# Kernel optimization log

Measured on AMD Instinct MI355X. Metric: run time of the kernel, lower is better.

## Reference

```python
import jax, jax.numpy as jnp
import numpy as np

D = 2048
N_EXPERTS = 64
K = 2


def setup_inputs() -> dict:
    key = jax.random.key(0)
    kx, kw = jax.random.split(key)
    x = jax.random.normal(kx, (4, 4096, D), dtype=jnp.float32)
    # xavier_uniform for Linear(d, n_experts): bound = sqrt(6/(fan_in+fan_out))
    bound = float(np.sqrt(6.0 / (D + N_EXPERTS)))
    W = jax.random.uniform(kw, (N_EXPERTS, D), dtype=jnp.float32, minval=-bound, maxval=bound)
    b = jnp.zeros((N_EXPERTS,), dtype=jnp.float32)
    return {"x": x, "W": W, "b": b}


def reference(x, W, b):
    # logits: [B, S, E]  (eval mode: no noise)
    logits = jnp.einsum("bsd,ed->bse", x, W) + b
    topk_vals, topk_idx = jax.lax.top_k(logits, K)  # [B, S, K]
    gates = jax.nn.softmax(topk_vals, axis=-1)
    return gates, topk_idx
```

## Files before the change

kernel.cpp:

```cpp
#include <hip/hip_runtime.h>
#include <math.h>

#define DD 2048
#define EE 64
#define TM 32
#define BK 64
#define NCHUNK (DD / BK)
#define THREADS 512

#define ROWB 272
#define XPLANE (TM * ROWB)
#define WPLANE (EE * ROWB)
#define BUFB   (XPLANE + WPLANE)

typedef _Float16 f16x8 __attribute__((ext_vector_type(8)));
typedef float    f32x4 __attribute__((ext_vector_type(4)));

#define BARRIER() { asm volatile("s_waitcnt lgkmcnt(0)" ::: "memory"); \
                    __builtin_amdgcn_s_barrier(); \
                    __builtin_amdgcn_sched_barrier(0); }

__device__ static inline void split8(const float4 a, const float4 b,
                                     f16x8& hi, f16x8& lo) {
    const float S = 32.f;
    const float v[8] = {a.x * S, a.y * S, a.z * S, a.w * S,
                        b.x * S, b.y * S, b.z * S, b.w * S};
#pragma unroll
    for (int i = 0; i < 8; ++i) {
        const _Float16 h = (_Float16)v[i];
        hi[i] = h;
        lo[i] = (_Float16)(v[i] - (float)h);
    }
}

__global__ __launch_bounds__(THREADS, 4) void router_kernel(
    const float* __restrict__ x, const float* __restrict__ W,
    const float* __restrict__ bias_g, float* __restrict__ out, int n_tokens)
{
    __shared__ __attribute__((aligned(16))) char  lds[2 * BUFB];
    __shared__ __attribute__((aligned(16))) float logits[TM * (EE + 1)];

    const int tid   = threadIdx.x;
    const int tBase = blockIdx.x * TM;

    const int sr = tid >> 3;
    const int sg = tid & 7;
    const bool do_x = (sr < TM);

    const float* xrow = x + (size_t)(tBase + (sr & (TM - 1))) * DD + sg * 8;
    const float* wrow = W + (size_t)sr * DD + sg * 8;

    float4 rxA0 = {0,0,0,0}, rxA1 = {0,0,0,0}, rwA0, rwA1;
    float4 rxB0 = {0,0,0,0}, rxB1 = {0,0,0,0}, rwB0, rwB1;

#define LOADS(c, rx0, rx1, rw0, rw1) { \
        rw0 = *(const float4*)&wrow[(c) * BK];       \
        rw1 = *(const float4*)&wrow[(c) * BK + 4];   \
        if (do_x) {                                  \
            rx0 = *(const float4*)&xrow[(c) * BK];   \
            rx1 = *(const float4*)&xrow[(c) * BK + 4]; } }

#define WRITE_STAGE(buf, rx0, rx1, rw0, rw1) { \
    char* base = lds + (size_t)(buf) * BUFB; \
    { f16x8 hi, lo; split8(rw0, rw1, hi, lo); \
      const int off = XPLANE + sr * ROWB + sg * 32; \
      *(f16x8*)(base + off)      = hi; \
      *(f16x8*)(base + off + 16) = lo; } \
    if (do_x) { f16x8 hi, lo; split8(rx0, rx1, hi, lo); \
      const int off = sr * ROWB + sg * 32; \
      *(f16x8*)(base + off)      = hi; \
      *(f16x8*)(base + off + 16) = lo; } }

    const int wv   = tid >> 6;
    const int lane = tid & 63;
    const int mt   = wv & 1;
    const int nt   = wv >> 1;
    const int r16  = lane & 15;
    const int kg   = lane >> 4;

    const int aoff = (mt * 16 + r16) * ROWB + kg * 32;
    const int boff = XPLANE + (nt * 16 + r16) * ROWB + kg * 32;

    f32x4 acc = {0.f, 0.f, 0.f, 0.f};

#define COMPUTE(buf) { \
    const char* base = lds + (size_t)(buf) * BUFB; \
    _Pragma("unroll") for (int ks = 0; ks < 2; ++ks) { \
        const f16x8 ah = *(const f16x8*)(base + aoff + ks * 128); \
        const f16x8 al = *(const f16x8*)(base + aoff + ks * 128 + 16); \
        const f16x8 bh = *(const f16x8*)(base + boff + ks * 128); \
        const f16x8 bl = *(const f16x8*)(base + boff + ks * 128 + 16); \
        acc = __builtin_amdgcn_mfma_f32_16x16x32_f16(ah, bh, acc, 0, 0, 0); \
        acc = __builtin_amdgcn_mfma_f32_16x16x32_f16(al, bh, acc, 0, 0, 0); \
        acc = __builtin_amdgcn_mfma_f32_16x16x32_f16(ah, bl, acc, 0, 0, 0); \
    } }

    LOADS(0, rxA0, rxA1, rwA0, rwA1);
    WRITE_STAGE(0, rxA0, rxA1, rwA0, rwA1);
    LOADS(1, rxB0, rxB1, rwB0, rwB1);

    for (int c = 0; c < NCHUNK; c += 2) {
        BARRIER();
        if (c + 2 < NCHUNK) LOADS(c + 2, rxA0, rxA1, rwA0, rwA1);
        COMPUTE(0);
        WRITE_STAGE(1, rxB0, rxB1, rwB0, rwB1);

        BARRIER();
        if (c + 3 < NCHUNK) LOADS(c + 3, rxB0, rxB1, rwB0, rwB1);
        COMPUTE(1);
        if (c + 2 < NCHUNK)
            WRITE_STAGE(0, rxA0, rxA1, rwA0, rwA1);
    }

    __syncthreads();
    const int col  = nt * 16 + r16;
    const float bcol = bias_g[col];
    const float INV  = 1.f / 1024.f;
    const int rbase  = mt * 16 + kg * 4;
#pragma unroll
    for (int r = 0; r < 4; ++r)
        logits[(rbase + r) * (EE + 1) + col] = acc[r] * INV + bcol;
    __syncthreads();

    if (tid < TM) {
        const float* lrow = &logits[tid * (EE + 1)];
        float v1 = -INFINITY, v2 = -INFINITY;
        int   i1 = 0, i2 = 0;
        for (int e = 0; e < EE; ++e) {
            const float v = lrow[e];
            if (v > v1) { v2 = v1; i2 = i1; v1 = v; i1 = e; }
            else if (v > v2) { v2 = v; i2 = e; }
        }
        const float ed  = expf(v2 - v1);
        const float inv = 1.f / (1.f + ed);
        const int tok = tBase + tid;
        out[tok * 2 + 0] = inv;
        out[tok * 2 + 1] = ed * inv;
        float* oidx = out + (size_t)2 * n_tokens;
        oidx[tok * 2 + 0] = (float)i1;
        oidx[tok * 2 + 1] = (float)i2;
    }
}

extern "C" void kernel_launch(void* const* d_in, const int* in_sizes, int n_in,
                              void* d_out, int out_size, void* d_ws, size_t ws_size,
                              hipStream_t stream) {
    const float* x = (const float*)d_in[0];
    const float* W = (const float*)d_in[1];
    const float* b = (const float*)d_in[2];
    float* out = (float*)d_out;

    const int n_tokens = in_sizes[0] / DD;
    const int n_blocks = n_tokens / TM;

    router_kernel<<<n_blocks, THREADS, 0, stream>>>(x, W, b, out, n_tokens);
}
```

Baseline: 202.8 us.

## Pre-split W into fp16 hi/lo in workspace and deepen load pipeline

A small pre-kernel converts W once per call into interleaved fp16 hi/lo pairs stored in the workspace. The router kernel then loads the pre-split W directly instead of re-splitting it in every block, and spreads the x loads across all 512 threads rather than half of them. The register pipeline also grows from two to three chunks in flight, with four barriers per iteration. The cost is an extra kernel launch and more registers, and the __syncthreads before the logits write is removed, which leans on the final barrier for ordering.

```diff
diff --git a/kernel.cpp b/kernel.cpp
--- a/kernel.cpp
+++ b/kernel.cpp
@@ -13,7 +13,10 @@
 #define WPLANE (EE * ROWB)
 #define BUFB   (XPLANE + WPLANE)
 
+#define WROWB 8192
+
 typedef _Float16 f16x8 __attribute__((ext_vector_type(8)));
+typedef _Float16 f16x4 __attribute__((ext_vector_type(4)));
 typedef float    f32x4 __attribute__((ext_vector_type(4)));
 
 #define BARRIER() { asm volatile("s_waitcnt lgkmcnt(0)" ::: "memory"); \
@@ -33,8 +36,32 @@
     }
 }
 
+__device__ static inline void split4(const float4 v, f16x4& hi, f16x4& lo) {
+    const float S = 32.f;
+    const float a0 = v.x * S, a1 = v.y * S, a2 = v.z * S, a3 = v.w * S;
+    const _Float16 h0 = (_Float16)a0, h1 = (_Float16)a1;
+    const _Float16 h2 = (_Float16)a2, h3 = (_Float16)a3;
+    hi = (f16x4){h0, h1, h2, h3};
+    lo = (f16x4){(_Float16)(a0 - (float)h0), (_Float16)(a1 - (float)h1),
+                 (_Float16)(a2 - (float)h2), (_Float16)(a3 - (float)h3)};
+}
+
+__global__ __launch_bounds__(256) void wsplit_kernel(
+    const float* __restrict__ W, char* __restrict__ wsp)
+{
+    const int gid = blockIdx.x * 256 + threadIdx.x;
+    const int e = gid >> 8, g = gid & 255;
+    const float4 a = *(const float4*)&W[(size_t)e * DD + g * 8];
+    const float4 b = *(const float4*)&W[(size_t)e * DD + g * 8 + 4];
+    f16x8 hi, lo;
+    split8(a, b, hi, lo);
+    char* dst = wsp + (size_t)e * WROWB + g * 32;
+    *(f16x8*)dst        = hi;
+    *(f16x8*)(dst + 16) = lo;
+}
+
 __global__ __launch_bounds__(THREADS, 4) void router_kernel(
-    const float* __restrict__ x, const float* __restrict__ W,
+    const float* __restrict__ x, const char* __restrict__ wsp,
     const float* __restrict__ bias_g, float* __restrict__ out, int n_tokens)
 {
     __shared__ __attribute__((aligned(16))) char  lds[2 * BUFB];
@@ -43,33 +70,30 @@
     const int tid   = threadIdx.x;
     const int tBase = blockIdx.x * TM;
 
-    const int sr = tid >> 3;
-    const int sg = tid & 7;
-    const bool do_x = (sr < TM);
+    const int swr = tid >> 3;
+    const int swg = tid & 7;
+    const char* wsrc = wsp + (size_t)swr * WROWB + swg * 32;
+    const int sxr = tid >> 4;
+    const int sxg = tid & 15;
+    const float* xsrc = x + (size_t)(tBase + sxr) * DD + sxg * 4;
 
-    const float* xrow = x + (size_t)(tBase + (sr & (TM - 1))) * DD + sg * 8;
-    const float* wrow = W + (size_t)sr * DD + sg * 8;
+    float4 xv0, xv1, xv2, xv3;
+    f16x8  wh0, wl0, wh1, wl1, wh2, wl2, wh3, wl3;
 
-    float4 rxA0 = {0,0,0,0}, rxA1 = {0,0,0,0}, rwA0, rwA1;
-    float4 rxB0 = {0,0,0,0}, rxB1 = {0,0,0,0}, rwB0, rwB1;
+#define LOADS(c, xv, wh, wl) { \
+    wh = *(const f16x8*)(wsrc + (c) * 256);        \
+    wl = *(const f16x8*)(wsrc + (c) * 256 + 16);   \
+    xv = *(const float4*)&xsrc[(c) * BK]; }
 
-#define LOADS(c, rx0, rx1, rw0, rw1) { \
-        rw0 = *(const float4*)&wrow[(c) * BK];       \
-        rw1 = *(const float4*)&wrow[(c) * BK + 4];   \
-        if (do_x) {                                  \
-            rx0 = *(const float4*)&xrow[(c) * BK];   \
-            rx1 = *(const float4*)&xrow[(c) * BK + 4]; } }
-
-#define WRITE_STAGE(buf, rx0, rx1, rw0, rw1) { \
+#define WRITE_STAGE(buf, xv, wh, wl) { \
     char* base = lds + (size_t)(buf) * BUFB; \
-    { f16x8 hi, lo; split8(rw0, rw1, hi, lo); \
-      const int off = XPLANE + sr * ROWB + sg * 32; \
-      *(f16x8*)(base + off)      = hi; \
-      *(f16x8*)(base + off + 16) = lo; } \
-    if (do_x) { f16x8 hi, lo; split8(rx0, rx1, hi, lo); \
-      const int off = sr * ROWB + sg * 32; \
-      *(f16x8*)(base + off)      = hi; \
-      *(f16x8*)(base + off + 16) = lo; } }
+    { f16x4 hi, lo; split4(xv, hi, lo); \
+      const int off = sxr * ROWB + (sxg >> 1) * 32 + (sxg & 1) * 8; \
+      *(f16x4*)(base + off)      = hi; \
+      *(f16x4*)(base + off + 16) = lo; } \
+    { const int off = XPLANE + swr * ROWB + swg * 32; \
+      *(f16x8*)(base + off)      = wh; \
+      *(f16x8*)(base + off + 16) = wl; } }
 
     const int wv   = tid >> 6;
     const int lane = tid & 63;
@@ -95,24 +119,33 @@
         acc = __builtin_amdgcn_mfma_f32_16x16x32_f16(ah, bl, acc, 0, 0, 0); \
     } }
 
-    LOADS(0, rxA0, rxA1, rwA0, rwA1);
-    WRITE_STAGE(0, rxA0, rxA1, rwA0, rwA1);
-    LOADS(1, rxB0, rxB1, rwB0, rwB1);
+    LOADS(0, xv0, wh0, wl0);
+    WRITE_STAGE(0, xv0, wh0, wl0);
+    LOADS(1, xv1, wh1, wl1);
+    LOADS(2, xv2, wh2, wl2);
 
-    for (int c = 0; c < NCHUNK; c += 2) {
+    for (int i = 0; i < NCHUNK; i += 4) {
         BARRIER();
-        if (c + 2 < NCHUNK) LOADS(c + 2, rxA0, rxA1, rwA0, rwA1);
+        if (i + 3 < NCHUNK) LOADS(i + 3, xv3, wh3, wl3);
         COMPUTE(0);
-        WRITE_STAGE(1, rxB0, rxB1, rwB0, rwB1);
+        if (i + 1 < NCHUNK) WRITE_STAGE(1, xv1, wh1, wl1);
 
         BARRIER();
-        if (c + 3 < NCHUNK) LOADS(c + 3, rxB0, rxB1, rwB0, rwB1);
+        if (i + 4 < NCHUNK) LOADS(i + 4, xv0, wh0, wl0);
         COMPUTE(1);
-        if (c + 2 < NCHUNK)
-            WRITE_STAGE(0, rxA0, rxA1, rwA0, rwA1);
+        if (i + 2 < NCHUNK) WRITE_STAGE(0, xv2, wh2, wl2);
+
+        BARRIER();
+        if (i + 5 < NCHUNK) LOADS(i + 5, xv1, wh1, wl1);
+        COMPUTE(0);
+        if (i + 3 < NCHUNK) WRITE_STAGE(1, xv3, wh3, wl3);
+
+        BARRIER();
+        if (i + 6 < NCHUNK) LOADS(i + 6, xv2, wh2, wl2);
+        COMPUTE(1);
+        if (i + 4 < NCHUNK) WRITE_STAGE(0, xv0, wh0, wl0);
     }
 
-    __syncthreads();
     const int col  = nt * 16 + r16;
     const float bcol = bias_g[col];
     const float INV  = 1.f / 1024.f;
@@ -153,5 +186,8 @@
     const int n_tokens = in_sizes[0] / DD;
     const int n_blocks = n_tokens / TM;
 
-    router_kernel<<<n_blocks, THREADS, 0, stream>>>(x, W, b, out, n_tokens);
+    char* wsp = (char*)d_ws;
+
+    wsplit_kernel<<<(EE * DD / 8) / 256, 256, 0, stream>>>(W, wsp);
+    router_kernel<<<n_blocks, THREADS, 0, stream>>>(x, wsp, b, out, n_tokens);
 }
```

Result: no change. 202.3 us (-0.2%).
